# Kernel tuning notes

Hardware: AMD Instinct MI355X
Metric: run time of the kernel (lower is better)

The kernel has to match this reference:

```python
import jax, jax.numpy as jnp
import numpy as np

N = 8192
D_FEAT = 1024
EPS = 1e-8


def setup_inputs() -> dict:
    key = jax.random.key(0)
    k1, k2 = jax.random.split(key)
    features = jax.random.normal(k1, (N, D_FEAT), dtype=jnp.float32)
    # nonnegative adjacency-like matrix (weights in [0,1))
    Mat = jax.random.uniform(k2, (N, N), dtype=jnp.float32)
    index = jnp.arange(N, dtype=jnp.int64)
    return {"features": features, "Mat": Mat, "index": index}


def reference(features, Mat, index):
    # Symmetric degree normalization: D^-1/2 A D^-1/2
    rowsum = Mat.sum(axis=1)                      # [N]
    d_inv_sqrt = (rowsum + EPS) ** -0.5
    d_inv_sqrt = jnp.where(jnp.isinf(d_inv_sqrt), 0.0, d_inv_sqrt)
    A_norm = Mat * d_inv_sqrt[:, None] * d_inv_sqrt[None, :]
    # GCN aggregation: spmm equivalent
    out = A_norm @ features                       # [N, d]
    # new_features[index] = out; rows not in index keep original features
    new_features = features.at[index].set(out)
    return new_features
```

## Files before the change

kernel.cpp:

```cpp
#include <hip/hip_runtime.h>


#define N_NODES 8192
#define D_FEAT  1024
#define GCN_EPS 1e-8f

typedef __attribute__((ext_vector_type(8))) short bf16x8;
typedef __attribute__((ext_vector_type(4))) float f32x4;
typedef __attribute__((ext_vector_type(4))) unsigned short u16x4;
typedef __attribute__((ext_vector_type(2))) unsigned int u32x2;

__device__ inline unsigned short f2bf(float x) {
  unsigned u = __float_as_uint(x);
  u += 0x7FFFu + ((u >> 16) & 1u);
  return (unsigned short)(u >> 16);
}

__device__ inline unsigned cvtpk(float lo, float hi) {
  unsigned r;
  asm("v_cvt_pk_bf16_f32 %0, %1, %2" : "=v"(r) : "v"(lo), "v"(hi));
  return r;
}

__device__ inline void async_copy16(const void* g, void* l) {
  __builtin_amdgcn_global_load_lds(
      (const __attribute__((address_space(1))) void*)g,
      (__attribute__((address_space(3))) void*)l,
      16, 0, 0);
}

__global__ __launch_bounds__(256) void rowsum(
    const float* __restrict__ Mat, float* __restrict__ dvec) {
  const int tid = threadIdx.x;
  const int lane = tid & 63, wave = tid >> 6;
  __shared__ float red[4];
#pragma unroll 1
  for (int rr = 0; rr < 4; ++rr) {
    const int row = blockIdx.x * 4 + rr;
    const f32x4* src = (const f32x4*)(Mat + (size_t)row * N_NODES);
    float s = 0.f;
#pragma unroll
    for (int i = 0; i < 8; ++i) {
      f32x4 v = src[tid + i * 256];
      s += (v.x + v.y) + (v.z + v.w);
    }
#pragma unroll
    for (int off = 32; off > 0; off >>= 1) s += __shfl_down(s, off);
    if (lane == 0) red[wave] = s;
    __syncthreads();
    if (tid == 0) {
      float t = (red[0] + red[1]) + (red[2] + red[3]);
      dvec[row] = 1.0f / sqrtf(t + GCN_EPS);
    }
    __syncthreads();
  }
}

__global__ __launch_bounds__(256) void scale_transpose(
    const float* __restrict__ F, const float* __restrict__ dvec,
    unsigned short* __restrict__ Fst) {
  __shared__ float tile[64][65];
  const int t = threadIdx.x;
  const int n0 = blockIdx.x * 64;
  const int j0 = blockIdx.y * 64;
  const int jr = t >> 4;
  const int c = t & 15;
#pragma unroll
  for (int i = 0; i < 4; ++i) {
    int jj = jr + 16 * i;
    float dv = dvec[j0 + jj];
    f32x4 v = *(const f32x4*)(F + (size_t)(j0 + jj) * D_FEAT + n0 + c * 4);
    tile[jj][c * 4 + 0] = v.x * dv;
    tile[jj][c * 4 + 1] = v.y * dv;
    tile[jj][c * 4 + 2] = v.z * dv;
    tile[jj][c * 4 + 3] = v.w * dv;
  }
  __syncthreads();
#pragma unroll
  for (int i = 0; i < 4; ++i) {
    int nn = jr + 16 * i;
    u16x4 o;
    o.x = f2bf(tile[c * 4 + 0][nn]);
    o.y = f2bf(tile[c * 4 + 1][nn]);
    o.z = f2bf(tile[c * 4 + 2][nn]);
    o.w = f2bf(tile[c * 4 + 3][nn]);
    *(u16x4*)(Fst + (size_t)(n0 + nn) * N_NODES + j0 + c * 4) = o;
  }
}

__global__ __launch_bounds__(256) void gemm_af32(
    const float* __restrict__ Mat,
    const unsigned short* __restrict__ Bt,
    const float* __restrict__ dvec,
    float* __restrict__ C) {
  const int K = N_NODES;
  __shared__ __align__(16) unsigned short As[128 * 32];
  __shared__ __align__(16) unsigned short Bs[128 * 32];

  const int tid = threadIdx.x;
  const int wave = tid >> 6, lane = tid & 63;
  const int slot = blockIdx.x;
  const int wg = (slot & 7) * 64 + (slot >> 3);
  const int tileM = (wg >> 3) * 128;
  const int tileN = (wg & 7) * 128;
  const int wm = (wave >> 1) * 64, wn = (wave & 1) * 64;
  const int lrow = lane & 15, quad = lane >> 4;

  const float* gA = Mat + (size_t)(tileM + (tid >> 3)) * K + (tid & 7) * 4;
  const unsigned short* gB0 = Bt + (size_t)(tileN + (tid >> 2)) * K + (tid & 3) * 8;
  const unsigned short* gB1 = Bt + (size_t)(tileN + 64 + (tid >> 2)) * K + (tid & 3) * 8;
  unsigned short* lB0 = &Bs[wave * 512];
  unsigned short* lB1 = &Bs[2048 + wave * 512];
  unsigned short* lA = &As[(tid >> 3) * 32 + (tid & 7) * 4];

  f32x4 acc[4][4] = {};

  for (int k0 = 0; k0 < K; k0 += 32) {
    __syncthreads();
    f32x4 a0 = *(const f32x4*)(gA + k0);
    f32x4 a1 = *(const f32x4*)(gA + k0 + (size_t)32 * K);
    f32x4 a2 = *(const f32x4*)(gA + k0 + (size_t)64 * K);
    f32x4 a3 = *(const f32x4*)(gA + k0 + (size_t)96 * K);
    async_copy16(gB0 + k0, lB0);
    async_copy16(gB1 + k0, lB1);
    u32x2 w;
    w.x = cvtpk(a0.x, a0.y); w.y = cvtpk(a0.z, a0.w); *(u32x2*)(lA + 0 * 1024) = w;
    w.x = cvtpk(a1.x, a1.y); w.y = cvtpk(a1.z, a1.w); *(u32x2*)(lA + 1 * 1024) = w;
    w.x = cvtpk(a2.x, a2.y); w.y = cvtpk(a2.z, a2.w); *(u32x2*)(lA + 2 * 1024) = w;
    w.x = cvtpk(a3.x, a3.y); w.y = cvtpk(a3.z, a3.w); *(u32x2*)(lA + 3 * 1024) = w;
    __syncthreads();

    bf16x8 af[4], bfr[4];
#pragma unroll
    for (int mi = 0; mi < 4; ++mi)
      af[mi] = *(const bf16x8*)&As[(wm + mi * 16 + lrow) * 32 + quad * 8];
#pragma unroll
    for (int ni = 0; ni < 4; ++ni)
      bfr[ni] = *(const bf16x8*)&Bs[(wn + ni * 16 + lrow) * 32 + quad * 8];
#pragma unroll
    for (int mi = 0; mi < 4; ++mi)
#pragma unroll
      for (int ni = 0; ni < 4; ++ni)
        acc[mi][ni] = __builtin_amdgcn_mfma_f32_16x16x32_bf16(
            af[mi], bfr[ni], acc[mi][ni], 0, 0, 0);
  }

#pragma unroll
  for (int mi = 0; mi < 4; ++mi) {
#pragma unroll
    for (int r = 0; r < 4; ++r) {
      int row = tileM + wm + mi * 16 + quad * 4 + r;
      float dv = dvec[row];
#pragma unroll
      for (int ni = 0; ni < 4; ++ni) {
        int col = tileN + wn + ni * 16 + lrow;
        C[(size_t)row * D_FEAT + col] = dv * acc[mi][ni][r];
      }
    }
  }
}

extern "C" void kernel_launch(void* const* d_in, const int* in_sizes, int n_in,
                              void* d_out, int out_size, void* d_ws, size_t ws_size,
                              hipStream_t stream) {
  const float* F = (const float*)d_in[0];
  const float* Mat = (const float*)d_in[1];
  float* out = (float*)d_out;

  char* ws = (char*)d_ws;
  float* dvec = (float*)ws;
  unsigned short* Fst = (unsigned short*)(ws + 32768);

  rowsum<<<N_NODES / 4, 256, 0, stream>>>(Mat, dvec);
  scale_transpose<<<dim3(D_FEAT / 64, N_NODES / 64), 256, 0, stream>>>(F, dvec, Fst);
  gemm_af32<<<512, 256, 0, stream>>>(Mat, Fst, dvec, out);
}
```

Baseline: 720.6 us.

## Load fp32 A tile directly to LDS asynchronously and swizzle LDS layouts

The A operand (Mat, fp32) is now copied straight into shared memory with global_load_lds instead of passing through registers, and the bf16 conversion moves to after the LDS read in each wave. Both the A and B LDS tiles get an XOR swizzle on the global source offsets to cut bank conflicts on the fragment reads. This frees registers and VALU work in the load phase, but doubles the LDS footprint for A and repeats the conversion work across waves that share the same rows.

```diff
diff --git a/kernel.cpp b/kernel.cpp
--- a/kernel.cpp
+++ b/kernel.cpp
@@ -8,7 +8,6 @@
 typedef __attribute__((ext_vector_type(8))) short bf16x8;
 typedef __attribute__((ext_vector_type(4))) float f32x4;
 typedef __attribute__((ext_vector_type(4))) unsigned short u16x4;
-typedef __attribute__((ext_vector_type(2))) unsigned int u32x2;
 
 __device__ inline unsigned short f2bf(float x) {
   unsigned u = __float_as_uint(x);
@@ -94,7 +93,7 @@
     const float* __restrict__ dvec,
     float* __restrict__ C) {
   const int K = N_NODES;
-  __shared__ __align__(16) unsigned short As[128 * 32];
+  __shared__ __align__(16) float Asf[128 * 32];
   __shared__ __align__(16) unsigned short Bs[128 * 32];
 
   const int tid = threadIdx.x;
@@ -106,37 +105,47 @@
   const int wm = (wave >> 1) * 64, wn = (wave & 1) * 64;
   const int lrow = lane & 15, quad = lane >> 4;
 
-  const float* gA = Mat + (size_t)(tileM + (tid >> 3)) * K + (tid & 7) * 4;
-  const unsigned short* gB0 = Bt + (size_t)(tileN + (tid >> 2)) * K + (tid & 3) * 8;
-  const unsigned short* gB1 = Bt + (size_t)(tileN + 64 + (tid >> 2)) * K + (tid & 3) * 8;
+  const int ass = ((tid & 7) ^ ((tid >> 3) & 7)) * 4;
+  const float* gA = Mat + (size_t)(tileM + (tid >> 3)) * K + ass;
+  float* lA = &Asf[wave * 256];
+
+  const int bss = ((tid & 3) ^ ((tid >> 2) & 3)) * 8;
+  const unsigned short* gB0 = Bt + (size_t)(tileN + (tid >> 2)) * K + bss;
+  const unsigned short* gB1 = Bt + (size_t)(tileN + 64 + (tid >> 2)) * K + bss;
   unsigned short* lB0 = &Bs[wave * 512];
   unsigned short* lB1 = &Bs[2048 + wave * 512];
-  unsigned short* lA = &As[(tid >> 3) * 32 + (tid & 7) * 4];
+
+  const int asub0 = ((quad * 2) ^ (lrow & 7)) * 4;
+  const int asub1 = ((quad * 2 + 1) ^ (lrow & 7)) * 4;
+  const int bsub = (quad ^ (lrow & 3)) * 8;
 
   f32x4 acc[4][4] = {};
 
   for (int k0 = 0; k0 < K; k0 += 32) {
     __syncthreads();
-    f32x4 a0 = *(const f32x4*)(gA + k0);
-    f32x4 a1 = *(const f32x4*)(gA + k0 + (size_t)32 * K);
-    f32x4 a2 = *(const f32x4*)(gA + k0 + (size_t)64 * K);
-    f32x4 a3 = *(const f32x4*)(gA + k0 + (size_t)96 * K);
+#pragma unroll
+    for (int p = 0; p < 4; ++p)
+      async_copy16(gA + k0 + (size_t)(32 * p) * K, lA + p * 1024);
     async_copy16(gB0 + k0, lB0);
     async_copy16(gB1 + k0, lB1);
-    u32x2 w;
-    w.x = cvtpk(a0.x, a0.y); w.y = cvtpk(a0.z, a0.w); *(u32x2*)(lA + 0 * 1024) = w;
-    w.x = cvtpk(a1.x, a1.y); w.y = cvtpk(a1.z, a1.w); *(u32x2*)(lA + 1 * 1024) = w;
-    w.x = cvtpk(a2.x, a2.y); w.y = cvtpk(a2.z, a2.w); *(u32x2*)(lA + 2 * 1024) = w;
-    w.x = cvtpk(a3.x, a3.y); w.y = cvtpk(a3.z, a3.w); *(u32x2*)(lA + 3 * 1024) = w;
     __syncthreads();
 
     bf16x8 af[4], bfr[4];
 #pragma unroll
-    for (int mi = 0; mi < 4; ++mi)
-      af[mi] = *(const bf16x8*)&As[(wm + mi * 16 + lrow) * 32 + quad * 8];
+    for (int mi = 0; mi < 4; ++mi) {
+      const float* ap = &Asf[(wm + mi * 16 + lrow) * 32];
+      f32x4 lo = *(const f32x4*)(ap + asub0);
+      f32x4 hi = *(const f32x4*)(ap + asub1);
+      union { unsigned u[4]; bf16x8 v; } pk;
+      pk.u[0] = cvtpk(lo.x, lo.y);
+      pk.u[1] = cvtpk(lo.z, lo.w);
+      pk.u[2] = cvtpk(hi.x, hi.y);
+      pk.u[3] = cvtpk(hi.z, hi.w);
+      af[mi] = pk.v;
+    }
 #pragma unroll
     for (int ni = 0; ni < 4; ++ni)
-      bfr[ni] = *(const bf16x8*)&Bs[(wn + ni * 16 + lrow) * 32 + quad * 8];
+      bfr[ni] = *(const bf16x8*)&Bs[(wn + ni * 16 + lrow) * 32 + bsub];
 #pragma unroll
     for (int mi = 0; mi < 4; ++mi)
 #pragma unroll
```

New measurement: 685.7 us. 1.05x faster.
